# Performance work log

Hardware: AMD Instinct MI355X
Metric: run time of the kernel (lower is better)

## Reference

```python
import jax, jax.numpy as jnp
import numpy as np

IDIM, CDIM, NUM_HEADS, N, M = 256, 512, 2, 128, 64
T, BSZ = 64, 128


def setup_inputs() -> dict:
    key = jax.random.key(0)
    ks = jax.random.split(key, 12)
    return {
        "embs": jax.random.normal(ks[0], (T, BSZ, IDIM), jnp.float32),
        "lens": jnp.clip(jax.random.randint(ks[1], (BSZ,), 0, 64), 1, T).astype(jnp.int32),
        "mem_bias": jax.random.normal(ks[2], (N, M), jnp.float32) * 0.05,
        "W_ih": jax.random.normal(ks[3], (4 * CDIM, IDIM + NUM_HEADS * M), jnp.float32) * 0.04,
        "W_hh": jax.random.normal(ks[4], (4 * CDIM, CDIM), jnp.float32) * 0.04,
        "b_ih": jnp.zeros((4 * CDIM,), jnp.float32),
        "b_hh": jnp.zeros((4 * CDIM,), jnp.float32),
        "Wr": jax.random.normal(ks[5], (NUM_HEADS, M + 6, CDIM), jnp.float32) * 0.04,
        "br": jnp.zeros((NUM_HEADS, M + 6), jnp.float32),
        "Ww": jax.random.normal(ks[6], (NUM_HEADS, 3 * M + 6, CDIM), jnp.float32) * 0.04,
        "bw": jnp.zeros((NUM_HEADS, 3 * M + 6), jnp.float32),
        "h0": jax.random.normal(ks[7], (CDIM,), jnp.float32) * 0.05,
        "c0": jax.random.normal(ks[8], (CDIM,), jnp.float32) * 0.05,
        "r0": jax.random.normal(ks[9], (NUM_HEADS, M), jnp.float32) * 0.02,
    }


def _address(mem, k, beta, g, s, gamma, w_prev):
    # mem: (b,N,M)  k:(b,M)  beta,g,gamma:(b,1)  s:(b,3)  w_prev:(b,N)
    beta = jax.nn.softplus(beta)
    g = jax.nn.sigmoid(g)
    s = jax.nn.softmax(s, axis=1)
    gamma = 1.0 + jax.nn.softplus(gamma)
    kk = k + 1e-16
    mm = mem + 1e-16
    dot = jnp.einsum('bnm,bm->bn', mm, kk)
    denom = jnp.linalg.norm(mm, axis=-1) * jnp.linalg.norm(kk, axis=-1, keepdims=True)
    sim = dot / jnp.maximum(denom, 1e-8)  # torch cosine_similarity eps
    wc = jax.nn.softmax(beta * sim, axis=1)
    wg = g * wc + (1.0 - g) * w_prev
    # circular convolution with 3-tap shift kernel: c[i]=s0*w[i-1]+s1*w[i]+s2*w[i+1]
    ww = (s[:, 0:1] * jnp.roll(wg, 1, axis=1)
          + s[:, 1:2] * wg
          + s[:, 2:3] * jnp.roll(wg, -1, axis=1))
    wp = ww ** gamma
    return wp / (jnp.sum(wp, axis=1, keepdims=True) + 1e-16)


def _split5(o):
    return o[:, :M], o[:, M:M + 1], o[:, M + 1:M + 2], o[:, M + 2:M + 5], o[:, M + 5:M + 6]


def _ntm_forward(embs, mem_bias, W_ih, W_hh, b_ih, b_hh, Wr, br, Ww, bw, h0, c0, r0):
    bsz = embs.shape[1]
    mem0 = jnp.broadcast_to(mem_bias, (bsz, N, M))
    reads0 = jnp.broadcast_to(r0[:, None, :], (NUM_HEADS, bsz, M))
    w0 = jnp.zeros((NUM_HEADS, bsz, N), embs.dtype)
    h = jnp.broadcast_to(h0, (bsz, CDIM))
    c = jnp.broadcast_to(c0, (bsz, CDIM))

    def step(carry, emb):
        h, c, mem, rw, wws, reads = carry
        x = jnp.concatenate([emb] + [reads[i] for i in range(NUM_HEADS)], axis=1)
        gates = x @ W_ih.T + h @ W_hh.T + (b_ih + b_hh)
        gi, gf, gg, go = jnp.split(gates, 4, axis=1)  # torch LSTM gate order i,f,g,o
        c = jax.nn.sigmoid(gf) * c + jax.nn.sigmoid(gi) * jnp.tanh(gg)
        h = jax.nn.sigmoid(go) * jnp.tanh(c)
        ctrl = h
        new_reads, new_rw, new_wws = [], [], []
        for hi in range(NUM_HEADS):  # head order: read_i then write_i, writes visible to later heads
            orh = ctrl @ Wr[hi].T + br[hi]
            k, beta, g, s, gamma = _split5(orh)
            w = _address(mem, k, beta, g, s, gamma, rw[hi])
            new_rw.append(w)
            new_reads.append(jnp.einsum('bn,bnm->bm', w, mem))
            owh = ctrl @ Ww[hi].T + bw[hi]
            k2, beta2, g2, s2, gamma2 = _split5(owh)
            e = jax.nn.sigmoid(owh[:, M + 6:2 * M + 6])
            a = owh[:, 2 * M + 6:3 * M + 6]
            w2 = _address(mem, k2, beta2, g2, s2, gamma2, wws[hi])
            mem = mem * (1.0 - w2[:, :, None] * e[:, None, :]) + w2[:, :, None] * a[:, None, :]
            new_wws.append(w2)
        o = jnp.concatenate([ctrl] + new_reads, axis=1)
        carry = (h, c, mem, jnp.stack(new_rw), jnp.stack(new_wws), jnp.stack(new_reads))
        return carry, (o, h, c)

    _, (os_, hs, cs) = jax.lax.scan(step, (h, c, mem0, w0, w0, reads0), embs)
    return os_, hs, cs  # (T,b,cdim+H*M), (T,b,cdim), (T,b,cdim)


def reference(embs, lens, mem_bias, W_ih, W_hh, b_ih, b_hh, Wr, br, Ww, bw, h0, c0, r0):
    os_, hs, cs = _ntm_forward(embs, mem_bias, W_ih, W_hh, b_ih, b_hh, Wr, br, Ww, bw, h0, c0, r0)
    bsz = embs.shape[1]
    bi = jnp.arange(bsz)
    h_fin = hs[lens - 1, bi][None]  # (1,b,cdim) final state at true sequence end
    c_fin = cs[lens - 1, bi][None]
    return os_, h_fin, c_fin
```

## Files before the change

kernel.cpp:

```cpp
#include <hip/hip_runtime.h>
#include <cmath>

#define WS_EMBT  0
#define WS_STATE 2097152
#define WS_C     2179072
#define WS_MEM   2244608
#define WS_RW    3293184
#define WS_WWS   3325952
#define WS_PART  3358720

#define GATES_LDS_BYTES ((3584 + 14336) * 4)

#define GLD16(g, l) __builtin_amdgcn_global_load_lds( \
    (const __attribute__((address_space(1))) void*)(g), \
    (__attribute__((address_space(3))) void*)(l), 16, 0, 0)

__device__ __forceinline__ float sigm(float x) { return 1.0f / (1.0f + expf(-x)); }
__device__ __forceinline__ float softplusf(float x) {
    return fmaxf(x, 0.0f) + log1pf(expf(-fabsf(x)));
}

__global__ __launch_bounds__(256) void k_embT(const float* __restrict__ embs,
                                              float* __restrict__ ws)
{
    int f4 = blockIdx.x * 256 + threadIdx.x;
    int k4 = f4 & 63, b = (f4 >> 6) & 127, t = f4 >> 13;
    float4 v = *(const float4*)&embs[(size_t)(t * 128 + b) * 256 + k4 * 4];
    *(float4*)&ws[WS_EMBT + ((size_t)(t * 64 + k4) * 128 + b) * 4] = v;
}

__global__ __launch_bounds__(256) void k_init(float* __restrict__ ws,
                                              const float* __restrict__ mem_bias,
                                              const float* __restrict__ h0,
                                              const float* __restrict__ c0,
                                              const float* __restrict__ r0)
{
    int i = blockIdx.x * 256 + threadIdx.x;
    if (i < 81920) {
        int ks = i >> 9, rem = i & 511, c4 = rem & 3;
        int k = ks * 4 + c4;
        ws[WS_STATE + i] = (ks < 32) ? r0[k] : h0[k - 128];
        return;
    }
    int j = i - 81920;
    if (j < 65536) { ws[WS_C + j] = c0[j >> 7]; return; }
    j -= 65536;
    if (j < 1048576) { ws[WS_MEM + j] = mem_bias[j & 8191]; return; }
    j -= 1048576;
    ws[WS_RW + j] = 0.0f;
}

__global__ void __launch_bounds__(256, 2) k_gates(
    const float* __restrict__ W_ih,
    const float* __restrict__ W_hh,
    const float* __restrict__ ws_c,
    float* __restrict__ partials,
    int t)
{
    extern __shared__ float sm[];
    float4* w_s4 = (float4*)sm;
    float4* x_s4 = (float4*)(sm + 3584);

    const int tx = threadIdx.x;
    const int rt = blockIdx.x >> 3, kz = blockIdx.x & 7;
    const int r0g = rt * 32, k0 = kz * 112;
    const int lane = tx & 63, wid = tx >> 6;

    const float* embsT  = ws_c + WS_EMBT + (size_t)t * 32768;
    const float* stateT = ws_c + WS_STATE;

#pragma unroll
    for (int it = 0; it < 3; ++it) {
        int f = it * 256 + tx;
        int rl = f / 28, kq = f - rl * 28;
        int kg = k0 + kq * 4, r = r0g + rl;
        const float* gp = (kg < 384) ? &W_ih[r * 384 + kg]
                                     : &W_hh[r * 512 + (kg - 384)];
        GLD16(gp, &w_s4[it * 256 + wid * 64]);
    }
    if (tx < 128) {
        int f = 768 + tx;
        int rl = f / 28, kq = f - rl * 28;
        int kg = k0 + kq * 4, r = r0g + rl;
        const float* gp = (kg < 384) ? &W_ih[r * 384 + kg]
                                     : &W_hh[r * 512 + (kg - 384)];
        GLD16(gp, &w_s4[768 + wid * 64]);
    }
#pragma unroll
    for (int it = 0; it < 14; ++it) {
        int f = it * 256 + tx;
        int k4g = kz * 28 + (f >> 7);
        int b = f & 127;
        const float* gp = (k4g < 64) ? &embsT[(size_t)k4g * 512 + b * 4]
                                     : &stateT[(size_t)(k4g - 64) * 512 + b * 4];
        GLD16(gp, &x_s4[it * 256 + wid * 64]);
    }
    __syncthreads();

    const int wr0 = wid * 8;
    float acc0[8] = {}, acc1[8] = {};
#pragma unroll 4
    for (int k4 = 0; k4 < 28; ++k4) {
        float4 xv0 = x_s4[k4 * 128 + lane];
        float4 xv1 = x_s4[k4 * 128 + 64 + lane];
#pragma unroll
        for (int r = 0; r < 8; ++r) {
            float4 wv = w_s4[(wr0 + r) * 28 + k4];
            acc0[r] += wv.x * xv0.x + wv.y * xv0.y + wv.z * xv0.z + wv.w * xv0.w;
            acc1[r] += wv.x * xv1.x + wv.y * xv1.y + wv.z * xv1.z + wv.w * xv1.w;
        }
    }
#pragma unroll
    for (int r = 0; r < 8; ++r) {
        int row = r0g + wr0 + r;
        partials[(size_t)kz * 262144 + row * 128 + lane]      = acc0[r];
        partials[(size_t)kz * 262144 + row * 128 + 64 + lane] = acc1[r];
    }
}

__global__ __launch_bounds__(256) void k_lstm(
    const float* __restrict__ partials,
    const float* __restrict__ b_ih,
    const float* __restrict__ b_hh,
    float* __restrict__ ws,
    float* __restrict__ d_out,
    const int* __restrict__ lens,
    int t)
{
    const int tx = threadIdx.x;
    const int half = blockIdx.x & 1, cht = blockIdx.x >> 1;
    const int ch = cht * 4 + (tx >> 6);
    const int lane = tx & 63, b = half * 64 + lane;

    float g4[4];
#pragma unroll
    for (int g = 0; g < 4; ++g) {
        int r = g * 512 + ch;
        float s = b_ih[r] + b_hh[r];
#pragma unroll
        for (int kzq = 0; kzq < 8; ++kzq)
            s += partials[(size_t)kzq * 262144 + r * 128 + b];
        g4[g] = s;
    }
    float* cp = ws + WS_C + ch * 128;
    float c_old = cp[b];
    float c_new = sigm(g4[1]) * c_old + sigm(g4[0]) * tanhf(g4[2]);
    float h_new = sigm(g4[3]) * tanhf(c_new);
    cp[b] = c_new;
    ws[WS_STATE + (32 + (ch >> 2)) * 512 + b * 4 + (ch & 3)] = h_new;
    d_out[((size_t)t * 128 + b) * 640 + ch] = h_new;
    if (lens[b] - 1 == t) {
        d_out[5242880 + b * 512 + ch] = h_new;
        d_out[5308416 + b * 512 + ch] = c_new;
    }
}

__global__ __launch_bounds__(256) void k_proj(
    const float* __restrict__ ws_c,
    const float* __restrict__ Wr,
    const float* __restrict__ Ww,
    float* __restrict__ part2)
{
    __shared__ float w_s[16 * 64];
    __shared__ float x_s[16 * 128 * 4];
    float4* w_s4 = (float4*)w_s;
    float4* x_s4 = (float4*)x_s;

    const int tx = threadIdx.x;
    const int jt = blockIdx.x >> 3, kz = blockIdx.x & 7;
    const int j0 = jt * 16, k0 = kz * 64;
    const float* stateT = ws_c + WS_STATE;

    {
        int rl = tx >> 4, kq = tx & 15;
        int j = j0 + rl;
        float4 v = make_float4(0.f, 0.f, 0.f, 0.f);
        if (j < 536) {
            int hi = j >= 268, q = j - hi * 268;
            v = (q < 70) ? *(const float4*)&Wr[(hi * 70 + q) * 512 + k0 + kq * 4]
                         : *(const float4*)&Ww[(hi * 198 + (q - 70)) * 512 + k0 + kq * 4];
        }
        w_s4[tx] = v;
    }
#pragma unroll
    for (int it = 0; it < 8; ++it) {
        int f = it * 256 + tx;
        int k4 = f >> 7, b = f & 127;
        x_s4[f] = *(const float4*)&stateT[(size_t)(32 + kz * 16 + k4) * 512 + b * 4];
    }
    __syncthreads();

    const int lane = tx & 63, wid = tx >> 6;
    const int jw0 = wid * 4;
    float acc0[4] = {}, acc1[4] = {};
#pragma unroll 4
    for (int k4 = 0; k4 < 16; ++k4) {
        float4 xv0 = x_s4[k4 * 128 + lane];
        float4 xv1 = x_s4[k4 * 128 + 64 + lane];
#pragma unroll
        for (int r = 0; r < 4; ++r) {
            float4 wv = w_s4[(jw0 + r) * 16 + k4];
            acc0[r] += wv.x * xv0.x + wv.y * xv0.y + wv.z * xv0.z + wv.w * xv0.w;
            acc1[r] += wv.x * xv1.x + wv.y * xv1.y + wv.z * xv1.z + wv.w * xv1.w;
        }
    }
#pragma unroll
    for (int r = 0; r < 4; ++r) {
        int j = j0 + jw0 + r;
        if (j < 536) {
            part2[(size_t)kz * 69632 + lane * 544 + j]        = acc0[r];
            part2[(size_t)kz * 69632 + (lane + 64) * 544 + j] = acc1[r];
        }
    }
}

__global__ __launch_bounds__(256) void k_memops(
    const float* __restrict__ part2,
    const float* __restrict__ br,
    const float* __restrict__ bw,
    float* __restrict__ ws,
    float* __restrict__ d_out,
    int t)
{
    const int b = blockIdx.x;
    const int tx = threadIdx.x;
    const int lx = tx & 127;
    const int grp = tx >> 7;
    const int wid = tx >> 6;

    __shared__ float mem_s[128 * 66];
    __shared__ float proj_s[544];
    __shared__ float wg2_s[2 * 128];
    __shared__ float wf_s[2 * 128];
    __shared__ float red_s[16];
    __shared__ float ea_s[128];
    __shared__ float rvp_s[4 * 66];

    float* memg   = ws + WS_MEM;
    float* stateT = ws + WS_STATE;
    float* rwg    = ws + WS_RW;
    float* wwsg   = ws + WS_WWS;

    for (int j = tx; j < 536; j += 256) {
        int hi = j >= 268, q = j - hi * 268;
        float s = (q < 70) ? br[hi * 70 + q] : bw[hi * 198 + (q - 70)];
#pragma unroll
        for (int kzq = 0; kzq < 8; ++kzq)
            s += part2[(size_t)kzq * 69632 + b * 544 + j];
        proj_s[j] = s;
    }
#pragma unroll
    for (int e = 0; e < 8; ++e) {
        int f4 = e * 256 + tx;
        int n = f4 >> 4, m4 = (f4 & 15) * 4;
        float4 v = *(const float4*)&memg[b * 8192 + f4 * 4];
        *(float2*)&mem_s[n * 66 + m4]     = make_float2(v.x, v.y);
        *(float2*)&mem_s[n * 66 + m4 + 2] = make_float2(v.z, v.w);
    }
    __syncthreads();

    for (int hi = 0; hi < 2; ++hi) {
        const float* p = proj_s + hi * 268 + grp * 70;
        float* wprev_g = (grp == 0 ? rwg : wwsg) + (hi * 128 + b) * 128;

        float beta = softplusf(p[64]);
        float g = sigm(p[65]);
        float s0 = p[66], s1 = p[67], s2 = p[68];
        float sm = fmaxf(s0, fmaxf(s1, s2));
        float e0 = expf(s0 - sm), e1 = expf(s1 - sm), e2 = expf(s2 - sm);
        float sden = e0 + e1 + e2;
        s0 = e0 / sden; s1 = e1 / sden; s2 = e2 / sden;
        float gamma = 1.0f + softplusf(p[69]);

        const float* mrow = mem_s + lx * 66;
        float dot = 0.f, nm = 0.f, nk = 0.f;
#pragma unroll
        for (int m = 0; m < 64; m += 2) {
            float2 kv2 = *(const float2*)&p[m];
            float2 mv2 = *(const float2*)&mrow[m];
            float kx = kv2.x + 1e-16f, ky = kv2.y + 1e-16f;
            float mx = mv2.x + 1e-16f, my = mv2.y + 1e-16f;
            dot += mx * kx + my * ky;
            nm  += mx * mx + my * my;
            nk  += kx * kx + ky * ky;
        }
        float sim = dot / fmaxf(sqrtf(nm) * sqrtf(nk), 1e-8f);
        float z = beta * sim;

        float r = z;
#pragma unroll
        for (int d = 32; d > 0; d >>= 1) r = fmaxf(r, __shfl_xor(r, d));
        if ((tx & 63) == 0) red_s[wid] = r;
        __syncthreads();
        float zmax = fmaxf(red_s[grp * 2], red_s[grp * 2 + 1]);
        float ez = expf(z - zmax);
        r = ez;
#pragma unroll
        for (int d = 32; d > 0; d >>= 1) r += __shfl_xor(r, d);
        if ((tx & 63) == 0) red_s[8 + wid] = r;
        __syncthreads();
        float zsum = red_s[8 + grp * 2] + red_s[8 + grp * 2 + 1];
        float wc = ez / zsum;
        float wgv = g * wc + (1.f - g) * wprev_g[lx];
        wg2_s[grp * 128 + lx] = wgv;
        __syncthreads();
        float wwv = s0 * wg2_s[grp * 128 + ((lx + 127) & 127)] + s1 * wgv
                  + s2 * wg2_s[grp * 128 + ((lx + 1) & 127)];
        float wp = powf(wwv, gamma);
        r = wp;
#pragma unroll
        for (int d = 32; d > 0; d >>= 1) r += __shfl_xor(r, d);
        if ((tx & 63) == 0) red_s[wid] = r;
        __syncthreads();
        float psum = red_s[grp * 2] + red_s[grp * 2 + 1];
        float wfin = wp / (psum + 1e-16f);
        wf_s[grp * 128 + lx] = wfin;
        wprev_g[lx] = wfin;
        __syncthreads();

        {
            int m = tx & 63, p4 = tx >> 6;
            float rv = 0.f;
            const int nb = p4 * 32;
#pragma unroll
            for (int n8 = 0; n8 < 32; ++n8) {
                int n = nb + n8;
                rv += wf_s[n] * mem_s[n * 66 + m];
            }
            rvp_s[p4 * 66 + m] = rv;
        }
        if (tx < 64)        ea_s[tx] = sigm(proj_s[hi * 268 + 140 + tx]);
        else if (tx < 128)  ea_s[tx] = proj_s[hi * 268 + 204 + (tx - 64)];
        __syncthreads();

        if (tx < 64) {
            float rvf = rvp_s[tx] + rvp_s[66 + tx] + rvp_s[132 + tx] + rvp_s[198 + tx];
            stateT[((hi * 64 + tx) >> 2) * 512 + b * 4 + (tx & 3)] = rvf;
            d_out[((size_t)t * 128 + b) * 640 + 512 + hi * 64 + tx] = rvf;
        }
#pragma unroll
        for (int e = 0; e < 16; ++e) {
            int f = e * 256 + tx;
            int n = f >> 5, m2 = (f & 31) * 2;
            float w2 = wf_s[128 + n];
            float2 mv = *(const float2*)&mem_s[n * 66 + m2];
            mv.x = mv.x * (1.f - w2 * ea_s[m2])     + w2 * ea_s[64 + m2];
            mv.y = mv.y * (1.f - w2 * ea_s[m2 + 1]) + w2 * ea_s[65 + m2];
            *(float2*)&mem_s[n * 66 + m2] = mv;
            if (hi == 1) *(float2*)&memg[b * 8192 + f * 2] = mv;
        }
        __syncthreads();
    }
}

extern "C" void kernel_launch(void* const* d_in, const int* in_sizes, int n_in,
                              void* d_out, int out_size, void* d_ws, size_t ws_size,
                              hipStream_t stream)
{
    (void)in_sizes; (void)n_in; (void)out_size; (void)ws_size;
    const float* embs     = (const float*)d_in[0];
    const int*   lens     = (const int*)  d_in[1];
    const float* mem_bias = (const float*)d_in[2];
    const float* W_ih     = (const float*)d_in[3];
    const float* W_hh     = (const float*)d_in[4];
    const float* b_ih     = (const float*)d_in[5];
    const float* b_hh     = (const float*)d_in[6];
    const float* Wr       = (const float*)d_in[7];
    const float* br       = (const float*)d_in[8];
    const float* Ww       = (const float*)d_in[9];
    const float* bw       = (const float*)d_in[10];
    const float* h0       = (const float*)d_in[11];
    const float* c0       = (const float*)d_in[12];
    const float* r0       = (const float*)d_in[13];
    float* out = (float*)d_out;
    float* ws  = (float*)d_ws;
    float* partials = ws + WS_PART;
    float* part2    = ws + WS_PART;

    hipFuncSetAttribute(reinterpret_cast<const void*>(&k_gates),
                        hipFuncAttributeMaxDynamicSharedMemorySize, GATES_LDS_BYTES);

    k_embT<<<2048, 256, 0, stream>>>(embs, ws);
    k_init<<<4928, 256, 0, stream>>>(ws, mem_bias, h0, c0, r0);
    for (int t = 0; t < 64; ++t) {
        k_gates<<<512, 256, GATES_LDS_BYTES, stream>>>(W_ih, W_hh, ws, partials, t);
        k_lstm<<<256, 256, 0, stream>>>(partials, b_ih, b_hh, ws, out, lens, t);
        k_proj<<<272, 256, 0, stream>>>(ws, Wr, Ww, part2);
        k_memops<<<128, 256, 0, stream>>>(part2, br, bw, ws, out, t);
    }
}
```

Baseline: 2.675 ms.

## Fuse LSTM cell, read/write head projection and memory ops into one per-batch kernel

Merges the LSTM cell update, the head projection GEMV and the memory addressing kernel into one kernel with one block per batch element. This cuts the kernels per timestep from four to two. The gate partials layout becomes batch-major so each block reads its own gates, and the C state moves to batch-major to match. The projection is now computed per batch with warp-shuffle reductions, so each block rereads all of Wr/Ww from global or L2 instead of sharing a tiled GEMM across blocks. It also runs on only 128 blocks.

```diff
diff --git a/kernel.cpp b/kernel.cpp
--- a/kernel.cpp
+++ b/kernel.cpp
@@ -43,7 +43,7 @@
         return;
     }
     int j = i - 81920;
-    if (j < 65536) { ws[WS_C + j] = c0[j >> 7]; return; }
+    if (j < 65536) { ws[WS_C + j] = c0[j & 511]; return; }
     j -= 65536;
     if (j < 1048576) { ws[WS_MEM + j] = mem_bias[j & 8191]; return; }
     j -= 1048576;
@@ -113,123 +113,33 @@
 #pragma unroll
     for (int r = 0; r < 8; ++r) {
         int row = r0g + wr0 + r;
-        partials[(size_t)kz * 262144 + row * 128 + lane]      = acc0[r];
-        partials[(size_t)kz * 262144 + row * 128 + 64 + lane] = acc1[r];
-    }
-}
-
-__global__ __launch_bounds__(256) void k_lstm(
+        partials[(size_t)kz * 262144 + lane * 2048 + row]        = acc0[r];
+        partials[(size_t)kz * 262144 + (lane + 64) * 2048 + row] = acc1[r];
+    }
+}
+
+__global__ __launch_bounds__(256) void k_fused(
     const float* __restrict__ partials,
     const float* __restrict__ b_ih,
     const float* __restrict__ b_hh,
-    float* __restrict__ ws,
-    float* __restrict__ d_out,
+    const float* __restrict__ Wr,
+    const float* __restrict__ br,
+    const float* __restrict__ Ww,
+    const float* __restrict__ bw,
     const int* __restrict__ lens,
-    int t)
-{
-    const int tx = threadIdx.x;
-    const int half = blockIdx.x & 1, cht = blockIdx.x >> 1;
-    const int ch = cht * 4 + (tx >> 6);
-    const int lane = tx & 63, b = half * 64 + lane;
-
-    float g4[4];
-#pragma unroll
-    for (int g = 0; g < 4; ++g) {
-        int r = g * 512 + ch;
-        float s = b_ih[r] + b_hh[r];
-#pragma unroll
-        for (int kzq = 0; kzq < 8; ++kzq)
-            s += partials[(size_t)kzq * 262144 + r * 128 + b];
-        g4[g] = s;
-    }
-    float* cp = ws + WS_C + ch * 128;
-    float c_old = cp[b];
-    float c_new = sigm(g4[1]) * c_old + sigm(g4[0]) * tanhf(g4[2]);
-    float h_new = sigm(g4[3]) * tanhf(c_new);
-    cp[b] = c_new;
-    ws[WS_STATE + (32 + (ch >> 2)) * 512 + b * 4 + (ch & 3)] = h_new;
-    d_out[((size_t)t * 128 + b) * 640 + ch] = h_new;
-    if (lens[b] - 1 == t) {
-        d_out[5242880 + b * 512 + ch] = h_new;
-        d_out[5308416 + b * 512 + ch] = c_new;
-    }
-}
-
-__global__ __launch_bounds__(256) void k_proj(
-    const float* __restrict__ ws_c,
-    const float* __restrict__ Wr,
-    const float* __restrict__ Ww,
-    float* __restrict__ part2)
-{
-    __shared__ float w_s[16 * 64];
-    __shared__ float x_s[16 * 128 * 4];
-    float4* w_s4 = (float4*)w_s;
-    float4* x_s4 = (float4*)x_s;
-
-    const int tx = threadIdx.x;
-    const int jt = blockIdx.x >> 3, kz = blockIdx.x & 7;
-    const int j0 = jt * 16, k0 = kz * 64;
-    const float* stateT = ws_c + WS_STATE;
-
-    {
-        int rl = tx >> 4, kq = tx & 15;
-        int j = j0 + rl;
-        float4 v = make_float4(0.f, 0.f, 0.f, 0.f);
-        if (j < 536) {
-            int hi = j >= 268, q = j - hi * 268;
-            v = (q < 70) ? *(const float4*)&Wr[(hi * 70 + q) * 512 + k0 + kq * 4]
-                         : *(const float4*)&Ww[(hi * 198 + (q - 70)) * 512 + k0 + kq * 4];
-        }
-        w_s4[tx] = v;
-    }
-#pragma unroll
-    for (int it = 0; it < 8; ++it) {
-        int f = it * 256 + tx;
-        int k4 = f >> 7, b = f & 127;
-        x_s4[f] = *(const float4*)&stateT[(size_t)(32 + kz * 16 + k4) * 512 + b * 4];
-    }
-    __syncthreads();
-
-    const int lane = tx & 63, wid = tx >> 6;
-    const int jw0 = wid * 4;
-    float acc0[4] = {}, acc1[4] = {};
-#pragma unroll 4
-    for (int k4 = 0; k4 < 16; ++k4) {
-        float4 xv0 = x_s4[k4 * 128 + lane];
-        float4 xv1 = x_s4[k4 * 128 + 64 + lane];
-#pragma unroll
-        for (int r = 0; r < 4; ++r) {
-            float4 wv = w_s4[(jw0 + r) * 16 + k4];
-            acc0[r] += wv.x * xv0.x + wv.y * xv0.y + wv.z * xv0.z + wv.w * xv0.w;
-            acc1[r] += wv.x * xv1.x + wv.y * xv1.y + wv.z * xv1.z + wv.w * xv1.w;
-        }
-    }
-#pragma unroll
-    for (int r = 0; r < 4; ++r) {
-        int j = j0 + jw0 + r;
-        if (j < 536) {
-            part2[(size_t)kz * 69632 + lane * 544 + j]        = acc0[r];
-            part2[(size_t)kz * 69632 + (lane + 64) * 544 + j] = acc1[r];
-        }
-    }
-}
-
-__global__ __launch_bounds__(256) void k_memops(
-    const float* __restrict__ part2,
-    const float* __restrict__ br,
-    const float* __restrict__ bw,
     float* __restrict__ ws,
     float* __restrict__ d_out,
     int t)
 {
     const int b = blockIdx.x;
     const int tx = threadIdx.x;
+    const int lane = tx & 63, wid = tx >> 6;
     const int lx = tx & 127;
     const int grp = tx >> 7;
-    const int wid = tx >> 6;
 
     __shared__ float mem_s[128 * 66];
     __shared__ float proj_s[544];
+    __shared__ float h_s[512];
     __shared__ float wg2_s[2 * 128];
     __shared__ float wf_s[2 * 128];
     __shared__ float red_s[16];
@@ -241,14 +151,6 @@
     float* rwg    = ws + WS_RW;
     float* wwsg   = ws + WS_WWS;
 
-    for (int j = tx; j < 536; j += 256) {
-        int hi = j >= 268, q = j - hi * 268;
-        float s = (q < 70) ? br[hi * 70 + q] : bw[hi * 198 + (q - 70)];
-#pragma unroll
-        for (int kzq = 0; kzq < 8; ++kzq)
-            s += part2[(size_t)kzq * 69632 + b * 544 + j];
-        proj_s[j] = s;
-    }
 #pragma unroll
     for (int e = 0; e < 8; ++e) {
         int f4 = e * 256 + tx;
@@ -256,6 +158,54 @@
         float4 v = *(const float4*)&memg[b * 8192 + f4 * 4];
         *(float2*)&mem_s[n * 66 + m4]     = make_float2(v.x, v.y);
         *(float2*)&mem_s[n * 66 + m4 + 2] = make_float2(v.z, v.w);
+    }
+
+    const float* pb = partials + (size_t)b * 2048;
+#pragma unroll
+    for (int cc = 0; cc < 2; ++cc) {
+        int ch = cc * 256 + tx;
+        float g4[4];
+#pragma unroll
+        for (int g = 0; g < 4; ++g) {
+            int r = g * 512 + ch;
+            float s = b_ih[r] + b_hh[r];
+#pragma unroll
+            for (int kz = 0; kz < 8; ++kz)
+                s += pb[(size_t)kz * 262144 + r];
+            g4[g] = s;
+        }
+        float* cp = ws + WS_C + b * 512 + ch;
+        float c_old = *cp;
+        float c_new = sigm(g4[1]) * c_old + sigm(g4[0]) * tanhf(g4[2]);
+        float h_new = sigm(g4[3]) * tanhf(c_new);
+        *cp = c_new;
+        h_s[ch] = h_new;
+        stateT[(32 + (ch >> 2)) * 512 + b * 4 + (ch & 3)] = h_new;
+        d_out[((size_t)t * 128 + b) * 640 + ch] = h_new;
+        if (lens[b] - 1 == t) {
+            d_out[5242880 + b * 512 + ch] = h_new;
+            d_out[5308416 + b * 512 + ch] = c_new;
+        }
+    }
+    __syncthreads();
+
+    {
+        const float4* h4 = (const float4*)h_s;
+        float4 hv0 = h4[lane];
+        float4 hv1 = h4[64 + lane];
+        for (int j = wid; j < 536; j += 4) {
+            int hi = j >= 268, q = j - hi * 268;
+            const float* wrow = (q < 70) ? &Wr[(size_t)(hi * 70 + q) * 512]
+                                         : &Ww[(size_t)(hi * 198 + (q - 70)) * 512];
+            float4 wv0 = ((const float4*)wrow)[lane];
+            float4 wv1 = ((const float4*)wrow)[64 + lane];
+            float d = wv0.x * hv0.x + wv0.y * hv0.y + wv0.z * hv0.z + wv0.w * hv0.w
+                    + wv1.x * hv1.x + wv1.y * hv1.y + wv1.z * hv1.z + wv1.w * hv1.w;
+#pragma unroll
+            for (int s = 32; s > 0; s >>= 1) d += __shfl_xor(d, s);
+            if (lane == 0)
+                proj_s[j] = d + ((q < 70) ? br[hi * 70 + q] : bw[hi * 198 + (q - 70)]);
+        }
     }
     __syncthreads();
 
@@ -375,7 +325,6 @@
     float* out = (float*)d_out;
     float* ws  = (float*)d_ws;
     float* partials = ws + WS_PART;
-    float* part2    = ws + WS_PART;
 
     hipFuncSetAttribute(reinterpret_cast<const void*>(&k_gates),
                         hipFuncAttributeMaxDynamicSharedMemorySize, GATES_LDS_BYTES);
@@ -384,8 +333,7 @@
     k_init<<<4928, 256, 0, stream>>>(ws, mem_bias, h0, c0, r0);
     for (int t = 0; t < 64; ++t) {
         k_gates<<<512, 256, GATES_LDS_BYTES, stream>>>(W_ih, W_hh, ws, partials, t);
-        k_lstm<<<256, 256, 0, stream>>>(partials, b_ih, b_hh, ws, out, lens, t);
-        k_proj<<<272, 256, 0, stream>>>(ws, Wr, Ww, part2);
-        k_memops<<<128, 256, 0, stream>>>(part2, br, bw, ws, out, t);
-    }
-}
+        k_fused<<<128, 256, 0, stream>>>(partials, b_ih, b_hh, Wr, br, Ww, bw,
+                                         lens, ws, out, t);
+    }
+}
```

Result: slower. 7.082 ms (+164.7%).
